# Optimization experiments

Hardware: AMD Instinct MI355X
Metric: run time of the kernel (lower is better)

Reference implementation:

```python
import jax, jax.numpy as jnp
from jax import lax
import numpy as np

# constants from module construction: segmentation_loss3D(alpha=1.0, percentile=95)
ALPHA_T = 1.0          # tversky alpha
BETA_T = 2.0 - ALPHA_T # tversky beta
EPS = 1e-5
HD_ALPHA = 2.0         # HausdorffDTLoss default alpha
BIG = 1e9              # stand-in for +inf in the min-plus distance transform


def _dt1d(f, axis):
    """Exact 1D squared Euclidean distance transform along `axis`:
    d[i] = min_j f[j] + (i - j)^2, computed as a min-plus scan over j."""
    n = f.shape[axis]
    fT = jnp.moveaxis(f, axis, 0)                      # (n, ...)
    idx = jnp.arange(n, dtype=f.dtype)
    d0 = jnp.full(fT.shape[1:] + (n,), BIG, f.dtype)   # (..., n)

    def step(d, xs):
        fj, j = xs
        return jnp.minimum(d, fj[..., None] + (idx - j) ** 2), None

    d, _ = lax.scan(step, d0, (fT, idx))
    return jnp.moveaxis(d, -1, axis)


def _edt(mask):
    """Euclidean distance to the nearest False voxel (matches scipy edt),
    over all axes except the two leading (stack, batch) axes."""
    f = jnp.where(mask, jnp.float32(BIG), jnp.float32(0.0))
    for ax in range(2, mask.ndim):
        f = _dt1d(f, ax)
    return jnp.sqrt(f)


def _distance_fields(pred, target_oh):
    # scipy loop runs edt over the full (C, X, Y, Z) array per batch element
    imgs = jnp.stack([pred, target_oh])           # (2, B, C, X, Y, Z)
    fg = imgs > 0.5
    masks = jnp.concatenate([fg, ~fg], axis=0)    # (4, B, C, X, Y, Z)
    dist = _edt(masks)
    field = dist[:2] + dist[2:]                   # fg_dist + bg_dist
    has_fg = jnp.any(fg, axis=(2, 3, 4, 5))       # (2, B) -- torch.no_grad guard
    field = jnp.where(has_fg[:, :, None, None, None, None], field, 0.0)
    field = lax.stop_gradient(field)
    return field[0], field[1]


def setup_inputs() -> dict:
    key = jax.random.key(0)
    k1, k2 = jax.random.split(key)
    B, C, X, Y, Z = 2, 8, 64, 64, 64
    inputs = jax.random.normal(k1, (B, C, X, Y, Z), dtype=jnp.float32)
    targets = jax.random.randint(k2, (B, X, Y, Z), 0, C, dtype=jnp.int32)
    return {"inputs": inputs, "targets": targets}


def reference(inputs, targets):
    C = inputs.shape[1]
    t_oh = jax.nn.one_hot(targets, C, axis=1, dtype=inputs.dtype)  # (B,C,X,Y,Z)

    # --- tversky (dice) loss ---
    probs = jax.nn.softmax(inputs, axis=1)
    red = tuple(range(2, inputs.ndim))
    tps = jnp.sum(probs * t_oh, red)
    fps = jnp.sum(probs * (1.0 - t_oh), red) * ALPHA_T
    fns = jnp.sum((1.0 - probs) * t_oh, red) * BETA_T
    score = 2.0 * tps / (2.0 * tps + fps + fns + EPS)   # (B, C)
    dice = 1.0 - jnp.mean(score, axis=0)[1:].mean()

    # --- cross entropy (mean over all voxels) ---
    logp = jax.nn.log_softmax(inputs, axis=1)
    ce = -jnp.mean(jnp.take_along_axis(logp, targets[:, None].astype(jnp.int32), axis=1))

    # --- Hausdorff distance-transform loss ---
    pred_dt, target_dt = _distance_fields(inputs, t_oh)
    pred_error = (inputs - t_oh) ** 2
    distance = pred_dt ** HD_ALPHA + target_dt ** HD_ALPHA
    hd = jnp.mean(pred_error * distance)

    return dice + ce + hd
```

## Files before the change

### kernel.cpp

```cpp
#include <hip/hip_runtime.h>

#define NVOX (64 * 64 * 64)
#define FM (16 * NVOX)



__global__ __launch_bounds__(256) void k_zy2(const float* __restrict__ in,
                                             const int* __restrict__ tg,
                                             float* __restrict__ f) {
    __shared__ float tA[64 * 65];
    __shared__ float tB[64 * 65];
    int blk = blockIdx.x;
    int src = blk >> 10;
    int s = blk & 1023;
    int b = s >> 9, c = (s >> 6) & 7, x = s & 63;
    int w = threadIdx.x >> 6;
    int z = threadIdx.x & 63;

    const float* pin = in + (b * 8 + c) * NVOX + x * 4096;
    const int* ptg = tg + b * NVOX + x * 4096;

    float dA[16], dB[16];
#pragma unroll
    for (int k = 0; k < 16; ++k) {
        int y = k * 4 + w;
        bool member;
        if (src == 0) member = pin[y * 64 + z] > 0.5f;
        else          member = ptg[y * 64 + z] == c;
        unsigned long long mkA = __ballot(!member);
        unsigned long long mkB = ~mkA;
        unsigned long long sfA = mkA << (63 - z), sbA = mkA >> z;
        int dfA = sfA ? __builtin_clzll(sfA) : 64;
        int dbA = sbA ? __builtin_ctzll(sbA) : 64;
        int da = dfA < dbA ? dfA : dbA;
        unsigned long long sfB = mkB << (63 - z), sbB = mkB >> z;
        int dfB = sfB ? __builtin_clzll(sfB) : 64;
        int dbB = sbB ? __builtin_ctzll(sbB) : 64;
        int db = dfB < dbB ? dfB : dbB;
        float a2 = (da > 63) ? 1e9f : (float)(da * da);
        float b2 = (db > 63) ? 1e9f : (float)(db * db);
        tA[y * 65 + z] = a2;
        tB[y * 65 + z] = b2;
        dA[k] = a2;
        dB[k] = b2;
    }
    __syncthreads();

    float* outA = f + (size_t)src * FM + (b * 8 + c) * NVOX + x * 4096;
    float* outB = f + (size_t)(src + 2) * FM + (b * 8 + c) * NVOX + x * 4096;
#pragma unroll
    for (int k = 0; k < 16; ++k) {
        int y = k * 4 + w;
        float d = dA[k];
        int q = 1;
        for (int dd = 1; dd <= 63 && (float)q < d; ++dd) {
            int jl = y - dd, jr = y + dd;
            float cl = (jl >= 0) ? tA[jl * 65 + z] : 1e9f;
            float cr = (jr < 64) ? tA[jr * 65 + z] : 1e9f;
            d = fminf(d, fminf(cl, cr) + (float)q);
            q += 2 * dd + 1;
        }
        outA[y * 64 + z] = fminf(d, 1e9f);
    }
#pragma unroll
    for (int k = 0; k < 16; ++k) {
        int y = k * 4 + w;
        float d = dB[k];
        int q = 1;
        for (int dd = 1; dd <= 63 && (float)q < d; ++dd) {
            int jl = y - dd, jr = y + dd;
            float cl = (jl >= 0) ? tB[jl * 65 + z] : 1e9f;
            float cr = (jr < 64) ? tB[jr * 65 + z] : 1e9f;
            d = fminf(d, fminf(cl, cr) + (float)q);
            q += 2 * dd + 1;
        }
        outB[y * 64 + z] = fminf(d, 1e9f);
    }
}

__global__ __launch_bounds__(256) void k_xdt(float* __restrict__ f) {
    __shared__ float tile[64 * 65];
    int blk = blockIdx.x;
    int m = blk >> 10;
    int s = blk & 1023;
    int b = s >> 9, c = (s >> 6) & 7, y = s & 63;
    int w = threadIdx.x >> 6;
    int z = threadIdx.x & 63;

    float* base = f + (size_t)m * FM + (b * 8 + c) * NVOX + y * 64;

    float d0_reg[16];
#pragma unroll
    for (int k = 0; k < 16; ++k) {
        int x = k * 4 + w;
        float v = base[x * 4096 + z];
        tile[x * 65 + z] = v;
        d0_reg[k] = v;
    }
    __syncthreads();

#pragma unroll
    for (int k = 0; k < 16; ++k) {
        int x = k * 4 + w;
        float d = d0_reg[k];
        int q = 1;
        for (int dd = 1; dd <= 63 && (float)q < d; ++dd) {
            int jl = x - dd, jr = x + dd;
            float cl = (jl >= 0) ? tile[jl * 65 + z] : 1e9f;
            float cr = (jr < 64) ? tile[jr * 65 + z] : 1e9f;
            d = fminf(d, fminf(cl, cr) + (float)q);
            q += 2 * dd + 1;
        }
        base[x * 4096 + z] = fminf(d, 1e9f);
    }
}

__global__ __launch_bounds__(256) void k_chds(const float* __restrict__ in,
                                              const int* __restrict__ tg,
                                              const float* __restrict__ f,
                                              float* __restrict__ statP,
                                              double* __restrict__ predS,
                                              double* __restrict__ tgtS) {
    __shared__ float part[4][27];
    __shared__ int af;
    if (threadIdx.x == 0) af = 0;
    __syncthreads();

    int blk = blockIdx.x;
    int v = blk * 256 + threadIdx.x;
    int b = v >> 18;
    int r = v & (NVOX - 1);
    int t = tg[v];
    int lane = threadIdx.x & 63;
    int wid = threadIdx.x >> 6;

    float xs[8];
#pragma unroll
    for (int c = 0; c < 8; ++c) xs[c] = in[(b * 8 + c) * NVOX + r];
    float mx = xs[0];
#pragma unroll
    for (int c = 1; c < 8; ++c) mx = fmaxf(mx, xs[c]);
    float se = 0.f;
#pragma unroll
    for (int c = 0; c < 8; ++c) se += expf(xs[c] - mx);
    float inv = 1.f / se;
    float lse = mx + logf(se);
    float xt = xs[0];
#pragma unroll
    for (int c = 1; c < 8; ++c) xt = (t == c) ? xs[c] : xt;

    bool anyP = false;
    float red[25];
#pragma unroll
    for (int c = 0; c < 8; ++c) {
        float p = expf(xs[c] - mx) * inv;
        red[c] = p;
        red[8 + c] = (t == c) ? p : 0.f;
        red[16 + c] = (t == c) ? 1.f : 0.f;
        anyP = anyP || (xs[c] > 0.5f);
    }
    red[24] = lse - xt;

#pragma unroll
    for (int k = 0; k < 25; ++k) {
        float s = red[k];
        s += __shfl_down(s, 32);
        s += __shfl_down(s, 16);
        s += __shfl_down(s, 8);
        s += __shfl_down(s, 4);
        s += __shfl_down(s, 2);
        s += __shfl_down(s, 1);
        red[k] = s;
    }
    bool wav = __any(anyP);
    if (lane == 0) {
#pragma unroll
        for (int k = 0; k < 25; ++k) part[wid][k] = red[k];
        if (wav) atomicOr(&af, 1);
    }

    float e2[8];
#pragma unroll
    for (int c = 0; c < 8; ++c) {
        float e = xs[c] - ((t == c) ? 1.f : 0.f);
        e2[c] = e * e;
    }
    float accP = 0.f, accT = 0.f;
#pragma unroll
    for (int m = 0; m < 4; ++m) {
        float fm[8];
#pragma unroll
        for (int c = 0; c < 8; ++c)
            fm[c] = f[(size_t)m * FM + (b * 8 + c) * NVOX + r];
        float am = 0.f;
#pragma unroll
        for (int i = 0; i < 8; ++i) {
            float d = 1e9f;
#pragma unroll
            for (int j = 0; j < 8; ++j)
                d = fminf(d, fm[j] + (float)((i - j) * (i - j)));
            am += e2[i] * d;
        }
        if (m & 1) accT += am; else accP += am;
    }
#pragma unroll
    for (int off = 32; off >= 1; off >>= 1) {
        accP += __shfl_down(accP, off);
        accT += __shfl_down(accT, off);
    }
    if (lane == 0) { part[wid][25] = accP; part[wid][26] = accT; }
    __syncthreads();

    int j = blk & 1023;
    if (threadIdx.x < 25)
        statP[(b * 26 + threadIdx.x) * 1024 + j] =
            part[0][threadIdx.x] + part[1][threadIdx.x] +
            part[2][threadIdx.x] + part[3][threadIdx.x];
    if (threadIdx.x == 25)
        statP[(b * 26 + 25) * 1024 + j] = af ? 1.f : 0.f;
    if (threadIdx.x == 26)
        predS[blk] = (double)part[0][25] + (double)part[1][25] +
                     (double)part[2][25] + (double)part[3][25];
    if (threadIdx.x == 27)
        tgtS[blk] = (double)part[0][26] + (double)part[1][26] +
                    (double)part[2][26] + (double)part[3][26];
}

__global__ __launch_bounds__(256) void k_final3(const float* __restrict__ statP,
                                                const double* __restrict__ predS,
                                                const double* __restrict__ tgtS,
                                                float* __restrict__ out) {
    __shared__ float rs[52];
    __shared__ double rd[4];
    int tid = threadIdx.x;
    int w = tid >> 6;
    int lane = tid & 63;

    for (int row = w; row < 52; row += 4) {
        const float* p = statP + row * 1024;
        float s = 0.f;
#pragma unroll
        for (int k = 0; k < 16; ++k) s += p[k * 64 + lane];
        s += __shfl_down(s, 32);
        s += __shfl_down(s, 16);
        s += __shfl_down(s, 8);
        s += __shfl_down(s, 4);
        s += __shfl_down(s, 2);
        s += __shfl_down(s, 1);
        if (lane == 0) rs[row] = s;
    }
    {
        const double* p = (w < 2) ? (predS + w * 1024) : (tgtS + (w - 2) * 1024);
        double s = 0.0;
#pragma unroll
        for (int k = 0; k < 16; ++k) s += p[k * 64 + lane];
        s += __shfl_down(s, 32);
        s += __shfl_down(s, 16);
        s += __shfl_down(s, 8);
        s += __shfl_down(s, 4);
        s += __shfl_down(s, 2);
        s += __shfl_down(s, 1);
        if (lane == 0) rd[w] = s;
    }
    __syncthreads();

    if (tid == 0) {
        bool fP0 = rs[0 * 26 + 25] > 0.f;
        bool fP1 = rs[1 * 26 + 25] > 0.f;
        double h = (fP0 ? rd[0] : 0.0) + (fP1 ? rd[1] : 0.0) + rd[2] + rd[3];
        float dsum = 0.f;
        for (int c = 1; c < 8; ++c) {
            float sc = 0.f;
            for (int b = 0; b < 2; ++b) {
                float S1 = rs[b * 26 + c];
                float S2 = rs[b * 26 + 8 + c];
                float Nc = rs[b * 26 + 16 + c];
                sc += 2.f * S2 / (2.f * S2 + (S1 - S2) + (Nc - S2) + 1e-5f);
            }
            dsum += sc * 0.5f;
        }
        float dice = 1.f - dsum / 7.f;
        float ce = (rs[0 * 26 + 24] + rs[1 * 26 + 24]) / 524288.f;
        out[0] = dice + ce + (float)(h / 4194304.0);
    }
}

__global__ __launch_bounds__(256, 4) void k_stats(const float* __restrict__ in,
                                                  const int* __restrict__ tg,
                                                  float* __restrict__ accF,
                                                  int* __restrict__ flags) {
    int r = blockIdx.x * 256 + threadIdx.x;
    int lane = threadIdx.x & 63;
    int wid = threadIdx.x >> 6;
    __shared__ float part[4][25];
    __shared__ int af;

    for (int b = 0; b < 2; ++b) {
        int t = tg[b * NVOX + r];
        float xs[8];
#pragma unroll
        for (int c = 0; c < 8; ++c) xs[c] = in[(b * 8 + c) * NVOX + r];
        float mx = xs[0];
#pragma unroll
        for (int c = 1; c < 8; ++c) mx = fmaxf(mx, xs[c]);
        float ex[8];
        float se = 0.f;
#pragma unroll
        for (int c = 0; c < 8; ++c) { ex[c] = expf(xs[c] - mx); se += ex[c]; }
        float inv = 1.f / se;
        float lse = mx + logf(se);
        float xt = xs[0];
#pragma unroll
        for (int c = 1; c < 8; ++c) xt = (t == c) ? xs[c] : xt;
        bool anyP = false;
        float red[25];
#pragma unroll
        for (int c = 0; c < 8; ++c) {
            float p = ex[c] * inv;
            red[c] = p;
            red[8 + c] = (t == c) ? p : 0.f;
            red[16 + c] = (t == c) ? 1.f : 0.f;
            anyP = anyP || (xs[c] > 0.5f);
        }
        red[24] = lse - xt;
#pragma unroll
        for (int k = 0; k < 25; ++k) {
            float s = red[k];
            s += __shfl_down(s, 32);
            s += __shfl_down(s, 16);
            s += __shfl_down(s, 8);
            s += __shfl_down(s, 4);
            s += __shfl_down(s, 2);
            s += __shfl_down(s, 1);
            red[k] = s;
        }
        if (threadIdx.x == 0) af = 0;
        __syncthreads();
        bool wav = __any(anyP);
        if (lane == 0) {
#pragma unroll
            for (int k = 0; k < 25; ++k) part[wid][k] = red[k];
            if (wav) atomicOr(&af, 1);
        }
        __syncthreads();
        if (threadIdx.x < 25) {
            float s = part[0][threadIdx.x] + part[1][threadIdx.x] +
                      part[2][threadIdx.x] + part[3][threadIdx.x];
            atomicAdd(&accF[b * 25 + threadIdx.x], s);
        }
        if (threadIdx.x == 0 && af) atomicOr(&flags[b], 1);
        __syncthreads();
    }
}

template <int M0>
__global__ __launch_bounds__(64) void k_mask_zy(const float* __restrict__ in,
                                                const int* __restrict__ tg,
                                                float* __restrict__ f) {
    __shared__ float tile[64 * 65];
    int blk = blockIdx.x;
    int m = M0 + (blk >> 10);
    int s = blk & 1023;
    int b = s >> 9, c = (s >> 6) & 7, x = s & 63;
    int tid = threadIdx.x;

    if ((m & 1) == 0) {
        const float* src = in + (b * 8 + c) * NVOX + x * 4096;
#pragma unroll 8
        for (int k = 0; k < 64; ++k) {
            bool fg = src[k * 64 + tid] > 0.5f;
            bool hot = (m < 2) ? fg : !fg;
            tile[k * 65 + tid] = hot ? 1e9f : 0.f;
        }
    } else {
        const int* src = tg + b * NVOX + x * 4096;
#pragma unroll 8
        for (int k = 0; k < 64; ++k) {
            bool fg = (src[k * 64 + tid] == c);
            bool hot = (m < 2) ? fg : !fg;
            tile[k * 65 + tid] = hot ? 1e9f : 0.f;
        }
    }
    __syncthreads();
    {
        float* row = &tile[tid * 65];
        float g = 1000.f;
#pragma unroll 8
        for (int z = 0; z < 64; ++z) {
            float v = row[z];
            g = (v == 0.f) ? 0.f : g + 1.f;
            row[z] = g;
        }
        g = 1000.f;
#pragma unroll 8
        for (int z = 63; z >= 0; --z) {
            float gf = row[z];
            g = (gf == 0.f) ? 0.f : g + 1.f;
            float d = fminf(gf, g);
            row[z] = (d > 63.f) ? 1e9f : d * d;
        }
    }
    __syncthreads();
    float* out = f + (size_t)(blk >> 10) * FM + (b * 8 + c) * NVOX + x * 4096;
    for (int i = 0; i < 64; ++i) {
        float d0 = tile[i * 65 + tid];
        float d = d0;
        int Ri = (int)sqrtf(d0) + 1;
        Ri = (Ri > 63) ? 63 : Ri;
        for (int dd = 1; dd <= Ri; ++dd) {
            float q = (float)(dd * dd);
            int jl = i - dd, jr = i + dd;
            float cl = (jl >= 0) ? tile[jl * 65 + tid] : 1e9f;
            float cr = (jr < 64) ? tile[jr * 65 + tid] : 1e9f;
            d = fminf(d, fminf(cl, cr) + q);
        }
        out[i * 64 + tid] = fminf(d, 1e9f);
    }
}

template <int M0>
__global__ __launch_bounds__(128, 4) void k_dtx(float* __restrict__ f) {
    __shared__ float wl[128 * 65];
    int blk = blockIdx.x;
    int mi = blk >> 9;
    int s = blk & 511;
    int plane = s >> 5;
    int y0 = (s & 31) * 2;
    int tid = threadIdx.x;
    float* fb = f + (size_t)mi * FM + plane * NVOX + y0 * 64;

#pragma unroll 8
    for (int j = 0; j < 64; ++j) wl[tid * 65 + j] = fb[j * 4096 + tid];

    float* row = &wl[tid * 65];
    for (int i = 0; i < 64; ++i) {
        float d0 = row[i];
        float d = d0;
        int Ri = (int)sqrtf(d0) + 1;
        Ri = (Ri > 63) ? 63 : Ri;
        for (int dd = 1; dd <= Ri; ++dd) {
            float q = (float)(dd * dd);
            int jl = i - dd, jr = i + dd;
            float cl = (jl >= 0) ? row[jl] : 1e9f;
            float cr = (jr < 64) ? row[jr] : 1e9f;
            d = fminf(d, fminf(cl, cr) + q);
        }
        fb[i * 4096 + tid] = fminf(d, 1e9f);
    }
}

template <int M0, int NM>
__global__ __launch_bounds__(256, 4) void k_cdt_hd(const float* __restrict__ in,
                                                   const int* __restrict__ tg,
                                                   const float* __restrict__ f,
                                                   const int* __restrict__ flags,
                                                   double* __restrict__ hd) {
    int v = blockIdx.x * 256 + threadIdx.x;
    int b = v >> 18;
    int r = v & (NVOX - 1);
    int t = tg[v];

    float e2[8];
#pragma unroll
    for (int c = 0; c < 8; ++c) {
        float e = in[(b * 8 + c) * NVOX + r] - ((t == c) ? 1.f : 0.f);
        e2[c] = e * e;
    }
    float acc = 0.f;
#pragma unroll
    for (int mi = 0; mi < NM; ++mi) {
        int m = M0 + mi;
        float fl = (m & 1) ? 1.f : (flags[b] ? 1.f : 0.f);
        float fm[8];
#pragma unroll
        for (int c = 0; c < 8; ++c)
            fm[c] = f[(size_t)mi * FM + (b * 8 + c) * NVOX + r];
        float am = 0.f;
#pragma unroll
        for (int i = 0; i < 8; ++i) {
            float d = 1e9f;
#pragma unroll
            for (int j = 0; j < 8; ++j)
                d = fminf(d, fm[j] + (float)((i - j) * (i - j)));
            am += e2[i] * d;
        }
        acc += fl * am;
    }
    float ssum = acc;
    ssum += __shfl_down(ssum, 32);
    ssum += __shfl_down(ssum, 16);
    ssum += __shfl_down(ssum, 8);
    ssum += __shfl_down(ssum, 4);
    ssum += __shfl_down(ssum, 2);
    ssum += __shfl_down(ssum, 1);
    __shared__ float part[4];
    int lane = threadIdx.x & 63;
    int wid = threadIdx.x >> 6;
    if (lane == 0) part[wid] = ssum;
    __syncthreads();
    if (threadIdx.x == 0)
        atomicAdd(hd, (double)(part[0] + part[1] + part[2] + part[3]));
}

__global__ void k_final(const float* __restrict__ accF,
                        const double* __restrict__ hd,
                        float* __restrict__ out) {
    float dsum = 0.f;
    for (int c = 1; c < 8; ++c) {
        float sc = 0.f;
        for (int b = 0; b < 2; ++b) {
            float S1 = accF[b * 25 + c];
            float S2 = accF[b * 25 + 8 + c];
            float Nc = accF[b * 25 + 16 + c];
            sc += 2.f * S2 / (2.f * S2 + (S1 - S2) + (Nc - S2) + 1e-5f);
        }
        dsum += sc * 0.5f;
    }
    float dice = 1.f - dsum / 7.f;
    float ce = (accF[24] + accF[25 + 24]) / 524288.f;
    float hdv = (float)(hd[0] / 4194304.0);
    out[0] = dice + ce + hdv;
}

template <int M0, int NM>
static void run_chunk(const float* in, const int* tg, float* f,
                      const int* flags, double* hd, hipStream_t stream) {
    k_mask_zy<M0><<<NM * 1024, 64, 0, stream>>>(in, tg, f);
    k_dtx<M0><<<NM * 512, 128, 0, stream>>>(f);
    k_cdt_hd<M0, NM><<<2048, 256, 0, stream>>>(in, tg, f, flags, hd);
}

extern "C" void kernel_launch(void* const* d_in, const int* in_sizes, int n_in,
                              void* d_out, int out_size, void* d_ws, size_t ws_size,
                              hipStream_t stream) {
    const float* in = (const float*)d_in[0];
    const int* tg = (const int*)d_in[1];
    float* out = (float*)d_out;
    float* f = (float*)d_ws;

    size_t offF = (size_t)4 * FM * 4;
    size_t need_fast = offF + 2048 * 8 * 2 + 52 * 1024 * 4;

    if (ws_size >= need_fast) {
        double* predS = (double*)((char*)d_ws + offF);
        double* tgtS = (double*)((char*)d_ws + offF + 16384);
        float* statP = (float*)((char*)d_ws + offF + 32768);
        k_zy2<<<2048, 256, 0, stream>>>(in, tg, f);
        k_xdt<<<4096, 256, 0, stream>>>(f);
        k_chds<<<2048, 256, 0, stream>>>(in, tg, f, statP, predS, tgtS);
        k_final3<<<1, 256, 0, stream>>>(statP, predS, tgtS, out);
    } else {
        size_t acc_off = ((ws_size - 256) / 256) * 256;
        char* accB = (char*)d_ws + acc_off;
        double* hd = (double*)accB;
        float* accF = (float*)(accB + 8);
        int* flags = (int*)(accB + 208);
        hipMemsetAsync(accB, 0, 256, stream);
        k_stats<<<1024, 256, 0, stream>>>(in, tg, accF, flags);
        int nm_cap = (int)(acc_off / ((size_t)FM * 4));
        if (nm_cap >= 2) {
            run_chunk<0, 2>(in, tg, f, flags, hd, stream);
            run_chunk<2, 2>(in, tg, f, flags, hd, stream);
        } else if (nm_cap >= 1) {
            run_chunk<0, 1>(in, tg, f, flags, hd, stream);
            run_chunk<1, 1>(in, tg, f, flags, hd, stream);
            run_chunk<2, 1>(in, tg, f, flags, hd, stream);
            run_chunk<3, 1>(in, tg, f, flags, hd, stream);
        }
        k_final<<<1, 1, 0, stream>>>(accF, hd, out);
    }
}
```

Measured before the change: 150.8 us.

## Pack fg/bg distance fields into 16-bit sum with membership bit

Stores the foreground and background partial distance transforms as a single 16-bit value (their sum, capped at 32767) plus a membership flag bit, instead of two separate float32 fields. This relies on exactly one of the two fields being nonzero per voxel, so each can be recovered from the sum and the flag. The change cuts intermediate workspace traffic by about 4x. It also halves the shared-memory tile use and the number of x-pass blocks, at the cost of serialising the two DT passes within each block. Distances above 32767 are clamped, which may change results when a class is absent, since the 1e9 sentinel is only restored for the exact value 32767.

```diff
diff --git a/kernel.cpp b/kernel.cpp
--- a/kernel.cpp
+++ b/kernel.cpp
@@ -1,15 +1,20 @@
 #include <hip/hip_runtime.h>
 
 #define NVOX (64 * 64 * 64)
+#define FMU (16 * NVOX)
 #define FM (16 * NVOX)
 
+
+__device__ __forceinline__ float unpack_val(unsigned short p) {
+    int v = p & 0x7fff;
+    return (v == 32767) ? 1e9f : (float)v;
+}
 
 
 __global__ __launch_bounds__(256) void k_zy2(const float* __restrict__ in,
                                              const int* __restrict__ tg,
-                                             float* __restrict__ f) {
-    __shared__ float tA[64 * 65];
-    __shared__ float tB[64 * 65];
+                                             unsigned short* __restrict__ f) {
+    __shared__ float tile[64 * 65];
     int blk = blockIdx.x;
     int src = blk >> 10;
     int s = blk & 1023;
@@ -21,12 +26,14 @@
     const int* ptg = tg + b * NVOX + x * 4096;
 
     float dA[16], dB[16];
+    bool mb[16];
 #pragma unroll
     for (int k = 0; k < 16; ++k) {
         int y = k * 4 + w;
         bool member;
         if (src == 0) member = pin[y * 64 + z] > 0.5f;
         else          member = ptg[y * 64 + z] == c;
+        mb[k] = member;
         unsigned long long mkA = __ballot(!member);
         unsigned long long mkB = ~mkA;
         unsigned long long sfA = mkA << (63 - z), sbA = mkA >> z;
@@ -39,15 +46,13 @@
         int db = dfB < dbB ? dfB : dbB;
         float a2 = (da > 63) ? 1e9f : (float)(da * da);
         float b2 = (db > 63) ? 1e9f : (float)(db * db);
-        tA[y * 65 + z] = a2;
-        tB[y * 65 + z] = b2;
+        tile[y * 65 + z] = a2;
         dA[k] = a2;
         dB[k] = b2;
     }
     __syncthreads();
 
-    float* outA = f + (size_t)src * FM + (b * 8 + c) * NVOX + x * 4096;
-    float* outB = f + (size_t)(src + 2) * FM + (b * 8 + c) * NVOX + x * 4096;
+    float rA[16];
 #pragma unroll
     for (int k = 0; k < 16; ++k) {
         int y = k * 4 + w;
@@ -55,13 +60,19 @@
         int q = 1;
         for (int dd = 1; dd <= 63 && (float)q < d; ++dd) {
             int jl = y - dd, jr = y + dd;
-            float cl = (jl >= 0) ? tA[jl * 65 + z] : 1e9f;
-            float cr = (jr < 64) ? tA[jr * 65 + z] : 1e9f;
+            float cl = (jl >= 0) ? tile[jl * 65 + z] : 1e9f;
+            float cr = (jr < 64) ? tile[jr * 65 + z] : 1e9f;
             d = fminf(d, fminf(cl, cr) + (float)q);
             q += 2 * dd + 1;
         }
-        outA[y * 64 + z] = fminf(d, 1e9f);
-    }
+        rA[k] = fminf(d, 1e9f);
+    }
+    __syncthreads();
+#pragma unroll
+    for (int k = 0; k < 16; ++k) tile[(k * 4 + w) * 65 + z] = dB[k];
+    __syncthreads();
+
+    unsigned short* out = f + (size_t)src * FMU + (b * 8 + c) * NVOX + x * 4096;
 #pragma unroll
     for (int k = 0; k < 16; ++k) {
         int y = k * 4 + w;
@@ -69,40 +80,50 @@
         int q = 1;
         for (int dd = 1; dd <= 63 && (float)q < d; ++dd) {
             int jl = y - dd, jr = y + dd;
-            float cl = (jl >= 0) ? tB[jl * 65 + z] : 1e9f;
-            float cr = (jr < 64) ? tB[jr * 65 + z] : 1e9f;
+            float cl = (jl >= 0) ? tile[jl * 65 + z] : 1e9f;
+            float cr = (jr < 64) ? tile[jr * 65 + z] : 1e9f;
             d = fminf(d, fminf(cl, cr) + (float)q);
             q += 2 * dd + 1;
         }
-        outB[y * 64 + z] = fminf(d, 1e9f);
-    }
-}
-
-__global__ __launch_bounds__(256) void k_xdt(float* __restrict__ f) {
+        float tot = rA[k] + fminf(d, 1e9f);
+        int vi = (int)fminf(tot, 32767.f);
+        out[y * 64 + z] = (unsigned short)((mb[k] ? 0x8000 : 0) | vi);
+    }
+}
+
+__global__ __launch_bounds__(256) void k_xdt(unsigned short* __restrict__ f) {
     __shared__ float tile[64 * 65];
     int blk = blockIdx.x;
-    int m = blk >> 10;
+    int src = blk >> 10;
     int s = blk & 1023;
     int b = s >> 9, c = (s >> 6) & 7, y = s & 63;
     int w = threadIdx.x >> 6;
     int z = threadIdx.x & 63;
 
-    float* base = f + (size_t)m * FM + (b * 8 + c) * NVOX + y * 64;
-
-    float d0_reg[16];
+    unsigned short* base = f + (size_t)src * FMU + (b * 8 + c) * NVOX + y * 64;
+
+    unsigned short pk[16];
+    float dA0[16], dB0[16];
 #pragma unroll
     for (int k = 0; k < 16; ++k) {
         int x = k * 4 + w;
-        float v = base[x * 4096 + z];
-        tile[x * 65 + z] = v;
-        d0_reg[k] = v;
-    }
-    __syncthreads();
-
+        unsigned short p = base[x * 4096 + z];
+        pk[k] = p;
+        float fv = unpack_val(p);
+        bool member = (p & 0x8000) != 0;
+        float a = member ? fv : 0.f;
+        float bb = member ? 0.f : fv;
+        tile[x * 65 + z] = a;
+        dA0[k] = a;
+        dB0[k] = bb;
+    }
+    __syncthreads();
+
+    float rA[16];
 #pragma unroll
     for (int k = 0; k < 16; ++k) {
         int x = k * 4 + w;
-        float d = d0_reg[k];
+        float d = dA0[k];
         int q = 1;
         for (int dd = 1; dd <= 63 && (float)q < d; ++dd) {
             int jl = x - dd, jr = x + dd;
@@ -111,13 +132,34 @@
             d = fminf(d, fminf(cl, cr) + (float)q);
             q += 2 * dd + 1;
         }
-        base[x * 4096 + z] = fminf(d, 1e9f);
+        rA[k] = fminf(d, 1e9f);
+    }
+    __syncthreads();
+#pragma unroll
+    for (int k = 0; k < 16; ++k) tile[(k * 4 + w) * 65 + z] = dB0[k];
+    __syncthreads();
+
+#pragma unroll
+    for (int k = 0; k < 16; ++k) {
+        int x = k * 4 + w;
+        float d = dB0[k];
+        int q = 1;
+        for (int dd = 1; dd <= 63 && (float)q < d; ++dd) {
+            int jl = x - dd, jr = x + dd;
+            float cl = (jl >= 0) ? tile[jl * 65 + z] : 1e9f;
+            float cr = (jr < 64) ? tile[jr * 65 + z] : 1e9f;
+            d = fminf(d, fminf(cl, cr) + (float)q);
+            q += 2 * dd + 1;
+        }
+        float tot = rA[k] + fminf(d, 1e9f);
+        int vi = (int)fminf(tot, 32767.f);
+        base[x * 4096 + z] = (unsigned short)((pk[k] & 0x8000) | vi);
     }
 }
 
 __global__ __launch_bounds__(256) void k_chds(const float* __restrict__ in,
                                               const int* __restrict__ tg,
-                                              const float* __restrict__ f,
+                                              const unsigned short* __restrict__ f,
                                               float* __restrict__ statP,
                                               double* __restrict__ predS,
                                               double* __restrict__ tgtS) {
@@ -187,21 +229,29 @@
     }
     float accP = 0.f, accT = 0.f;
 #pragma unroll
-    for (int m = 0; m < 4; ++m) {
-        float fm[8];
-#pragma unroll
-        for (int c = 0; c < 8; ++c)
-            fm[c] = f[(size_t)m * FM + (b * 8 + c) * NVOX + r];
+    for (int src = 0; src < 2; ++src) {
+        float fmA[8], fmB[8];
+#pragma unroll
+        for (int c = 0; c < 8; ++c) {
+            unsigned short p = f[(size_t)src * FMU + (b * 8 + c) * NVOX + r];
+            float fv = unpack_val(p);
+            bool member = (p & 0x8000) != 0;
+            fmA[c] = member ? fv : 0.f;
+            fmB[c] = member ? 0.f : fv;
+        }
         float am = 0.f;
 #pragma unroll
         for (int i = 0; i < 8; ++i) {
-            float d = 1e9f;
-#pragma unroll
-            for (int j = 0; j < 8; ++j)
-                d = fminf(d, fm[j] + (float)((i - j) * (i - j)));
-            am += e2[i] * d;
-        }
-        if (m & 1) accT += am; else accP += am;
+            float da = 1e9f, db = 1e9f;
+#pragma unroll
+            for (int j = 0; j < 8; ++j) {
+                float q = (float)((i - j) * (i - j));
+                da = fminf(da, fmA[j] + q);
+                db = fminf(db, fmB[j] + q);
+            }
+            am += e2[i] * (da + db);
+        }
+        if (src) accT += am; else accP += am;
     }
 #pragma unroll
     for (int off = 32; off >= 1; off >>= 1) {
@@ -536,20 +586,21 @@
     const float* in = (const float*)d_in[0];
     const int* tg = (const int*)d_in[1];
     float* out = (float*)d_out;
-    float* f = (float*)d_ws;
-
-    size_t offF = (size_t)4 * FM * 4;
-    size_t need_fast = offF + 2048 * 8 * 2 + 52 * 1024 * 4;
+
+    size_t offF = (size_t)2 * FMU * 2;
+    size_t need_fast = offF + 16384 + 16384 + 52 * 1024 * 4;
 
     if (ws_size >= need_fast) {
+        unsigned short* fu = (unsigned short*)d_ws;
         double* predS = (double*)((char*)d_ws + offF);
         double* tgtS = (double*)((char*)d_ws + offF + 16384);
         float* statP = (float*)((char*)d_ws + offF + 32768);
-        k_zy2<<<2048, 256, 0, stream>>>(in, tg, f);
-        k_xdt<<<4096, 256, 0, stream>>>(f);
-        k_chds<<<2048, 256, 0, stream>>>(in, tg, f, statP, predS, tgtS);
+        k_zy2<<<2048, 256, 0, stream>>>(in, tg, fu);
+        k_xdt<<<2048, 256, 0, stream>>>(fu);
+        k_chds<<<2048, 256, 0, stream>>>(in, tg, fu, statP, predS, tgtS);
         k_final3<<<1, 256, 0, stream>>>(statP, predS, tgtS, out);
     } else {
+        float* f = (float*)d_ws;
         size_t acc_off = ((ws_size - 256) / 256) * 256;
         char* accB = (char*)d_ws + acc_off;
         double* hd = (double*)accB;
```

Result: faster. 144.3 us (-4.3%).
